# Optimization experiments

Hardware: AMD Instinct MI355X
Metric: run time of the kernel (lower is better)

The kernel has to match this reference:

```python
import jax, jax.numpy as jnp
import numpy as np

B, S, H, NH, L, MLP_MULT = 4, 1024, 1024, 16, 2, 4
DK = H // NH
EPS = 1e-5


def setup_inputs() -> dict:
    key = jax.random.key(0)
    ks = jax.random.split(key, 8)
    p = lambda k, shape: jax.random.normal(k, shape, dtype=jnp.float32) * 0.02
    return {
        'hidden_states': jax.random.normal(ks[0], (B, S, H), dtype=jnp.float32),
        'attn_w': p(ks[1], (L, H, 3 * H)),
        'attn_b': jnp.zeros((L, 3 * H), jnp.float32),
        'proj_w': p(ks[2], (L, H, H)),
        'proj_b': jnp.zeros((L, H), jnp.float32),
        'fc_w': p(ks[3], (L, H, MLP_MULT * H)),
        'fc_b': jnp.zeros((L, MLP_MULT * H), jnp.float32),
        'fc2_w': p(ks[4], (L, MLP_MULT * H, H)),
        'fc2_b': jnp.zeros((L, H), jnp.float32),
        'ln1_g': jnp.ones((L, H), jnp.float32),
        'ln1_b': jnp.zeros((L, H), jnp.float32),
        'ln2_g': jnp.ones((L, H), jnp.float32),
        'ln2_b': jnp.zeros((L, H), jnp.float32),
        'position_ids': jnp.arange(S, dtype=jnp.int32),
    }


def _ln(x, g, b):
    m = jnp.mean(x, axis=-1, keepdims=True)
    v = jnp.var(x, axis=-1, keepdims=True)
    return (x - m) * jax.lax.rsqrt(v + EPS) * g + b


def _rotate_half(x):
    x1, x2 = jnp.split(x, 2, axis=-1)
    return jnp.concatenate((-x2, x1), axis=-1)


def _forward(hidden_states, attn_w, attn_b, proj_w, proj_b, fc_w, fc_b,
             fc2_w, fc2_b, ln1_g, ln1_b, ln2_g, ln2_b, position_ids):
    # rotary tables (fp32 math, as in RotaryEmbedding.forward)
    inv_freq = 1.0 / (10000.0 ** (jnp.arange(0, DK, 2, dtype=jnp.float32) / DK))
    freqs = position_ids.astype(jnp.float32)[:, None] * inv_freq[None, :]  # [S, DK/2]
    emb = jnp.concatenate((freqs, freqs), axis=-1)                          # [S, DK]
    cos = jnp.cos(emb)[None, None]  # [1,1,S,DK]
    sin = jnp.sin(emb)[None, None]
    causal = jnp.tril(jnp.ones((S, S), dtype=bool))
    neg = jnp.finfo(jnp.float32).min
    scale = 1.0 / np.sqrt(DK).astype(np.float32)

    h = hidden_states
    for i in range(L):
        # attention block
        x = _ln(h, ln1_g[i], ln1_b[i])
        qkv = x @ attn_w[i] + attn_b[i]                  # Conv1D c_attn
        q, k, v = jnp.split(qkv, 3, axis=-1)
        heads = lambda t: t.reshape(B, S, NH, DK).transpose(0, 2, 1, 3)
        q, k, v = heads(q), heads(k), heads(v)           # [B,NH,S,DK]
        q = q * cos + _rotate_half(q) * sin
        k = k * cos + _rotate_half(k) * sin
        # fp32 QK^T (baddbmm with alpha=scale, beta=0)
        w = jnp.einsum('bhqd,bhkd->bhqk', q.astype(jnp.float32),
                       k.astype(jnp.float32)) * scale    # [B,NH,S,S]
        w = jnp.where(causal, w, neg)
        w = jax.nn.softmax(w, axis=-1).astype(v.dtype)   # attn dropout is identity (eval)
        a = jnp.einsum('bhqk,bhkd->bhqd', w, v)
        a = a.transpose(0, 2, 1, 3).reshape(B, S, H)     # merge_heads
        h = h + (a @ proj_w[i] + proj_b[i])              # c_proj + residual
        # MLP block (gelu_new == tanh-approx gelu)
        x = _ln(h, ln2_g[i], ln2_b[i])
        mid = jax.nn.gelu(x @ fc_w[i] + fc_b[i], approximate=True)
        h = h + (mid @ fc2_w[i] + fc2_b[i])
    return h


def reference(hidden_states, attn_w, attn_b, proj_w, proj_b, fc_w, fc_b,
              fc2_w, fc2_b, ln1_g, ln1_b, ln2_g, ln2_b, position_ids):
    return _forward(hidden_states, attn_w, attn_b, proj_w, proj_b, fc_w, fc_b,
                    fc2_w, fc2_b, ln1_g, ln1_b, ln2_g, ln2_b, position_ids)
```

## Files before the change

### kernel.cpp

```cpp
#include <hip/hip_runtime.h>

#define B_ 4
#define S_ 1024
#define H_ 1024
#define NH_ 16
#define DK_ 64
#define MLPH_ 4096
#define EPS_ 1e-5f

typedef __attribute__((ext_vector_type(8))) short short8_t;
typedef __attribute__((ext_vector_type(8))) unsigned short ushort8_t;
typedef __attribute__((ext_vector_type(4))) float f32x4;

__device__ __forceinline__ unsigned short f2bf(float f) {
  unsigned int u = __float_as_uint(f);
  u = u + 0x7fffu + ((u >> 16) & 1u);
  return (unsigned short)(u >> 16);
}
__device__ __forceinline__ float bf2f(unsigned short b) {
  return __uint_as_float(((unsigned int)b) << 16);
}

__device__ __forceinline__ void gload16(const void* g, void* l) {
  typedef const __attribute__((address_space(1))) unsigned int GU;
  typedef __attribute__((address_space(3))) unsigned int LU;
  __builtin_amdgcn_global_load_lds((GU*)(size_t)g, (LU*)(unsigned int)(size_t)l, 16, 0, 0);
}

__device__ __forceinline__ float gelu_tanh(float x) {
  float y = 1.5957691216057308f * (x + 0.044715f * x * x * x);
  return x / (1.0f + __expf(-y));
}

__global__ __launch_bounds__(256) void rope_tab_init(const int* __restrict__ pos,
                                                     float2* __restrict__ tab) {
  int idx = blockIdx.x * 256 + threadIdx.x;
  int d2 = idx & 31, s = idx >> 5;
  float invf = __expf(-0.2878231366242557f * (float)d2);
  float th = (float)pos[s] * invf;
  float sn, cs;
  __sincosf(th, &sn, &cs);
  tab[idx] = make_float2(cs, sn);
}

__global__ __launch_bounds__(256) void wconv(const float* __restrict__ src0,
                                             unsigned short* __restrict__ dst0,
                                             int K, int N) {
  __shared__ float t[32][33];
  const float* src = src0 + (size_t)blockIdx.z * K * N;
  unsigned short* dst = dst0 + (size_t)blockIdx.z * N * K;
  int n0 = blockIdx.x * 32, k0 = blockIdx.y * 32;
  int tid = threadIdx.x;
  int r = tid >> 3, c = (tid & 7) * 4;
  const float* s = src + (size_t)(k0 + r) * N + n0 + c;
  float4 v = *(const float4*)s;
  t[r][c] = v.x; t[r][c + 1] = v.y; t[r][c + 2] = v.z; t[r][c + 3] = v.w;
  __syncthreads();
  ushort4 o;
  o.x = f2bf(t[c + 0][r]); o.y = f2bf(t[c + 1][r]);
  o.z = f2bf(t[c + 2][r]); o.w = f2bf(t[c + 3][r]);
  *(ushort4*)(dst + (size_t)(n0 + r) * K + k0 + c) = o;
}

__global__ __launch_bounds__(256) void ln_kernel(const float* __restrict__ x,
                                                 const float* __restrict__ g,
                                                 const float* __restrict__ b,
                                                 unsigned short* __restrict__ y) {
  int row = blockIdx.x, tid = threadIdx.x;
  const float* xp = x + (size_t)row * H_;
  float4 v = *((const float4*)xp + tid);
  float s  = v.x + v.y + v.z + v.w;
  float s2 = v.x * v.x + v.y * v.y + v.z * v.z + v.w * v.w;
  #pragma unroll
  for (int o = 1; o < 64; o <<= 1) {
    s  += __shfl_xor(s, o, 64);
    s2 += __shfl_xor(s2, o, 64);
  }
  __shared__ float r1[4], r2[4];
  if ((tid & 63) == 0) { r1[tid >> 6] = s; r2[tid >> 6] = s2; }
  __syncthreads();
  s  = r1[0] + r1[1] + r1[2] + r1[3];
  s2 = r2[0] + r2[1] + r2[2] + r2[3];
  float mean = s * (1.0f / H_);
  float var  = s2 * (1.0f / H_) - mean * mean;
  float inv  = rsqrtf(var + EPS_);
  float4 gv = *((const float4*)g + tid);
  float4 bv = *((const float4*)b + tid);
  ushort4 o;
  o.x = f2bf((v.x - mean) * inv * gv.x + bv.x);
  o.y = f2bf((v.y - mean) * inv * gv.y + bv.y);
  o.z = f2bf((v.z - mean) * inv * gv.z + bv.z);
  o.w = f2bf((v.w - mean) * inv * gv.w + bv.w);
  *(ushort4*)(y + (size_t)row * H_ + tid * 4) = o;
}

template <int MODE, int NT>
__global__ __launch_bounds__(256) void gemm_mfma(
    const unsigned short* __restrict__ A, const unsigned short* __restrict__ Bt,
    const float* __restrict__ bias, const float* __restrict__ resid,
    void* __restrict__ outp, int M, int N, int K, const float2* __restrict__ rtab) {
  constexpr int BN = NT * 32;
  constexpr int CB = BN / 32;
  __shared__ __align__(16) unsigned short As[2][128 * 64];
  __shared__ __align__(16) unsigned short Bs[2][BN * 64];
  int tid = threadIdx.x;
  int w = tid >> 6, lane = tid & 63;
  int gx = gridDim.x;
  int bid = blockIdx.y * gx + blockIdx.x;
  int xcd = bid & 7, r = bid >> 3;
  int rw = gx >> 1;
  int ry = xcd >> 1, rx = xcd & 1;
  int lm = r / rw, ln = r % rw;
  int m0 = (ry * (gridDim.y >> 2) + lm) * 128;
  int n0 = (rx * rw + ln) * BN;
  int wr = w >> 1, wc = w & 1;
  int fr = lane & 15, kg = lane >> 4;
  f32x4 acc[4][NT];
  #pragma unroll
  for (int m = 0; m < 4; m++)
    #pragma unroll
    for (int n = 0; n < NT; n++) {
      acc[m][n][0] = 0.f; acc[m][n][1] = 0.f; acc[m][n][2] = 0.f; acc[m][n][3] = 0.f;
    }
  int srow = lane >> 3;
  int scol = ((lane & 7) ^ srow) * 8;
  const unsigned short* Ap = A  + (size_t)(m0 + w * 32 + srow) * K + scol;
  const unsigned short* Bp = Bt + (size_t)(n0 + w * (8 * CB) + srow) * K + scol;
  int sx = (fr & 7);
  int nk = K >> 6;
  {
    char* AsB = (char*)As[0] + w * 4096;
    char* BsB = (char*)Bs[0] + w * CB * 1024;
    #pragma unroll
    for (int i = 0; i < 4; i++) gload16(Ap + (size_t)i * 8 * K, AsB + i * 1024);
    #pragma unroll
    for (int i = 0; i < CB; i++) gload16(Bp + (size_t)i * 8 * K, BsB + i * 1024);
  }
  __syncthreads();
  for (int t = 0; t < nk; t++) {
    int cur = t & 1;
    if (t + 1 < nk) {
      const unsigned short* Ap2 = Ap + (size_t)(t + 1) * 64;
      const unsigned short* Bp2 = Bp + (size_t)(t + 1) * 64;
      char* AsB = (char*)As[cur ^ 1] + w * 4096;
      char* BsB = (char*)Bs[cur ^ 1] + w * CB * 1024;
      #pragma unroll
      for (int i = 0; i < 4; i++) gload16(Ap2 + (size_t)i * 8 * K, AsB + i * 1024);
      #pragma unroll
      for (int i = 0; i < CB; i++) gload16(Bp2 + (size_t)i * 8 * K, BsB + i * 1024);
    }
    #pragma unroll
    for (int kk = 0; kk < 2; kk++) {
      int slot = ((kk * 4 + kg) ^ sx) << 4;
      short8_t af[4], bfr[NT];
      #pragma unroll
      for (int m = 0; m < 4; m++)
        af[m] = *(const short8_t*)((char*)As[cur] + (wr * 64 + m * 16 + fr) * 128 + slot);
      #pragma unroll
      for (int n = 0; n < NT; n++)
        bfr[n] = *(const short8_t*)((char*)Bs[cur] + (wc * (NT * 16) + n * 16 + fr) * 128 + slot);
      #pragma unroll
      for (int m = 0; m < 4; m++)
        #pragma unroll
        for (int n = 0; n < NT; n++)
          acc[m][n] = __builtin_amdgcn_mfma_f32_16x16x32_bf16(af[m], bfr[n], acc[m][n], 0, 0, 0);
    }
    __syncthreads();
  }

  if (MODE == 3) {
    int seg = n0 >> 10;
    if (seg < 2) {
      #pragma unroll
      for (int n = 0; n < 2; n++) {
        int col0 = n0 + wc * 64 + n * 16 + fr;
        int d2 = n * 16 + fr;
        float bv0 = bias[col0], bv2 = bias[col0 + 32];
        #pragma unroll
        for (int m = 0; m < 4; m++) {
          int row = m0 + wr * 64 + m * 16 + kg * 4;
          #pragma unroll
          for (int r2 = 0; r2 < 4; r2++) {
            int s = (row + r2) & (S_ - 1);
            float2 cssn = rtab[(s << 5) + d2];
            float a0 = acc[m][n][r2] + bv0;
            float a2 = acc[m][n + 2][r2] + bv2;
            size_t base = (size_t)(row + r2) * N;
            ((unsigned short*)outp)[base + col0]      = f2bf(a0 * cssn.x - a2 * cssn.y);
            ((unsigned short*)outp)[base + col0 + 32] = f2bf(a2 * cssn.x + a0 * cssn.y);
          }
        }
      }
    } else {
      #pragma unroll
      for (int n = 0; n < NT; n++) {
        int col = n0 + wc * (NT * 16) + n * 16 + fr;
        float bv = bias[col];
        #pragma unroll
        for (int m = 0; m < 4; m++) {
          int row = m0 + wr * 64 + m * 16 + kg * 4;
          #pragma unroll
          for (int r2 = 0; r2 < 4; r2++)
            ((unsigned short*)outp)[(size_t)(row + r2) * N + col] = f2bf(acc[m][n][r2] + bv);
        }
      }
    }
    return;
  }
  #pragma unroll
  for (int n = 0; n < NT; n++) {
    int col = n0 + wc * (NT * 16) + n * 16 + fr;
    float bv = bias[col];
    #pragma unroll
    for (int m = 0; m < 4; m++) {
      int row = m0 + wr * 64 + m * 16 + kg * 4;
      #pragma unroll
      for (int r2 = 0; r2 < 4; r2++) {
        float v = acc[m][n][r2] + bv;
        size_t idx = (size_t)(row + r2) * N + col;
        if (MODE == 2)      ((float*)outp)[idx] = resid[idx] + v;
        else if (MODE == 1) ((unsigned short*)outp)[idx] = f2bf(gelu_tanh(v));
        else                ((unsigned short*)outp)[idx] = f2bf(v);
      }
    }
  }
}

__global__ __launch_bounds__(256) void attn9(const unsigned short* __restrict__ qkv,
                                             unsigned short* __restrict__ aout) {
  __shared__ __align__(16) unsigned short Ks[2][64 * 64];
  __shared__ __align__(16) unsigned short Vt[2][64 * 64];
  __shared__ __align__(16) unsigned short Ps[4][16 * 64];
  const float SCL2 = 0.18033688011112443f;
  const float THR2 = 11.541560327111708f;
  int tid = threadIdx.x;
  int w = tid >> 6, lane = tid & 63;
  int fr = lane & 15, kg = lane >> 4;
  int lid = ((blockIdx.z << 4) + blockIdx.y) * 16 + blockIdx.x;
  int phase = lid >> 8, s256 = lid & 255;
  int i = s256 >> 6, combo = s256 & 63;
  int qt;
  if (phase == 0)      qt = 15 - i;
  else if (phase == 1) qt = i;
  else if (phase == 2) qt = 11 - i;
  else                 qt = 4 + i;
  int head = combo & 15, b = combo >> 4;
  int q0 = qt * 64;
  const unsigned short* base = qkv + ((size_t)b * S_) * 3072 + head * 64;

  const unsigned short* qp = base + (size_t)(q0 + w * 16 + fr) * 3072 + kg * 8;
  short8_t qa0 = *(const short8_t*)qp;
  short8_t qa1 = *(const short8_t*)(qp + 32);

  f32x4 acc[4];
  float mrun = -3.0e38f, lrun = 0.f;
  #pragma unroll
  for (int n = 0; n < 4; n++) {
    acc[n][0] = 0.f; acc[n][1] = 0.f; acc[n][2] = 0.f; acc[n][3] = 0.f;
  }

  int skv = lane;
  int sd0 = w * 16;
  int qrow = q0 + w * 16 + fr;

  const unsigned short* kp0 = base + 1024 + (size_t)skv * 3072 + sd0;
  short8_t ka = *(const short8_t*)kp0;
  short8_t kb = *(const short8_t*)(kp0 + 8);
  short8_t va = *(const short8_t*)(kp0 + 1024);
  short8_t vb = *(const short8_t*)(kp0 + 1032);

  int ntiles = qt + 1;
  for (int t = 0; t < ntiles; t++) {
    int cur = t & 1;
    {
      unsigned kbyte = skv * 128 + sd0 * 2;
      unsigned ksw = (skv & 7) << 4;
      *(short8_t*)((char*)Ks[cur] + (kbyte ^ ksw)) = ka;
      *(short8_t*)((char*)Ks[cur] + ((kbyte + 16) ^ ksw)) = kb;
      #pragma unroll
      for (int j = 0; j < 8; j++) {
        int d0 = sd0 + j, d1 = sd0 + 8 + j;
        *(unsigned short*)((char*)Vt[cur] + ((d0 * 128 + skv * 2) ^ ((d0 & 7) << 4))) = (unsigned short)va[j];
        *(unsigned short*)((char*)Vt[cur] + ((d1 * 128 + skv * 2) ^ ((d1 & 7) << 4))) = (unsigned short)vb[j];
      }
    }
    if (t + 1 < ntiles) {
      const unsigned short* kp = base + 1024 + (size_t)((t + 1) * 64 + skv) * 3072 + sd0;
      ka = *(const short8_t*)kp;
      kb = *(const short8_t*)(kp + 8);
      va = *(const short8_t*)(kp + 1024);
      vb = *(const short8_t*)(kp + 1032);
    }
    __syncthreads();
    short8_t b0[4], b1[4], v0[4], v1[4];
    #pragma unroll
    for (int n = 0; n < 4; n++) {
      int kvrow = n * 16 + fr;
      unsigned sw = (kvrow & 7) << 4;
      b0[n] = *(const short8_t*)((char*)Ks[cur] + ((kvrow * 128 + kg * 16) ^ sw));
      b1[n] = *(const short8_t*)((char*)Ks[cur] + ((kvrow * 128 + 64 + kg * 16) ^ sw));
    }
    #pragma unroll
    for (int n = 0; n < 4; n++) {
      int d = n * 16 + fr;
      unsigned sw = (d & 7) << 4;
      v0[n] = *(const short8_t*)((char*)Vt[cur] + ((d * 128 + kg * 16) ^ sw));
      v1[n] = *(const short8_t*)((char*)Vt[cur] + ((d * 128 + 64 + kg * 16) ^ sw));
    }
    f32x4 st[4];
    __builtin_amdgcn_s_setprio(1);
    #pragma unroll
    for (int n = 0; n < 4; n++) {
      f32x4 z; z[0] = 0.f; z[1] = 0.f; z[2] = 0.f; z[3] = 0.f;
      z = __builtin_amdgcn_mfma_f32_16x16x32_bf16(b0[n], qa0, z, 0, 0, 0);
      z = __builtin_amdgcn_mfma_f32_16x16x32_bf16(b1[n], qa1, z, 0, 0, 0);
      st[n] = z;
    }
    __builtin_amdgcn_s_setprio(0);
    bool diag = (t == qt);
    float rm = -3.0e38f;
    #pragma unroll
    for (int n = 0; n < 4; n++)
      #pragma unroll
      for (int j = 0; j < 4; j++) {
        float sv = st[n][j] * SCL2;
        if (diag && (t * 64 + n * 16 + kg * 4 + j > qrow)) sv = -1.0e30f;
        st[n][j] = sv;
        rm = fmaxf(rm, sv);
      }
    if (__any(rm > mrun + THR2)) {
      rm = fmaxf(rm, __shfl_xor(rm, 16, 64));
      rm = fmaxf(rm, __shfl_xor(rm, 32, 64));
      float mn = fmaxf(mrun, rm);
      float sc = exp2f(mrun - mn);
      mrun = mn;
      lrun *= sc;
      #pragma unroll
      for (int n = 0; n < 4; n++) {
        acc[n][0] *= sc; acc[n][1] *= sc; acc[n][2] *= sc; acc[n][3] *= sc;
      }
    }
    {
      float ls = 0.f;
      #pragma unroll
      for (int n = 0; n < 4; n++) {
        float e0 = exp2f(st[n][0] - mrun);
        float e1 = exp2f(st[n][1] - mrun);
        float e2 = exp2f(st[n][2] - mrun);
        float e3 = exp2f(st[n][3] - mrun);
        ls += (e0 + e1) + (e2 + e3);
        unsigned lo, hi;
        asm("v_cvt_pk_bf16_f32 %0, %1, %2" : "=v"(lo) : "v"(e0), "v"(e1));
        asm("v_cvt_pk_bf16_f32 %0, %1, %2" : "=v"(hi) : "v"(e2), "v"(e3));
        uint2 pk; pk.x = lo; pk.y = hi;
        *(uint2*)((char*)Ps[w] + ((fr * 128 + n * 32 + kg * 8) ^ ((fr & 7) << 4))) = pk;
      }
      lrun += ls;
    }
    asm volatile("s_waitcnt lgkmcnt(0)" ::: "memory");
    unsigned psw = (fr & 7) << 4;
    short8_t pa0 = *(const short8_t*)((char*)Ps[w] + ((fr * 128 + kg * 16) ^ psw));
    short8_t pa1 = *(const short8_t*)((char*)Ps[w] + ((fr * 128 + 64 + kg * 16) ^ psw));
    __builtin_amdgcn_s_setprio(1);
    #pragma unroll
    for (int n = 0; n < 4; n++) {
      acc[n] = __builtin_amdgcn_mfma_f32_16x16x32_bf16(v0[n], pa0, acc[n], 0, 0, 0);
      acc[n] = __builtin_amdgcn_mfma_f32_16x16x32_bf16(v1[n], pa1, acc[n], 0, 0, 0);
    }
    __builtin_amdgcn_s_setprio(0);
  }
  {
    float ls = lrun;
    ls += __shfl_xor(ls, 16, 64);
    ls += __shfl_xor(ls, 32, 64);
    float inv = 1.0f / ls;
    size_t row = (size_t)b * S_ + q0 + w * 16 + fr;
    unsigned short* op = aout + row * H_ + head * 64 + kg * 4;
    #pragma unroll
    for (int n = 0; n < 4; n++) {
      ushort4 o;
      o.x = f2bf(acc[n][0] * inv);
      o.y = f2bf(acc[n][1] * inv);
      o.z = f2bf(acc[n][2] * inv);
      o.w = f2bf(acc[n][3] * inv);
      *(ushort4*)(op + n * 16) = o;
    }
  }
}

extern "C" void kernel_launch(void* const* d_in, const int* in_sizes, int n_in,
                              void* d_out, int out_size, void* d_ws, size_t ws_size,
                              hipStream_t stream) {
  const float* hs     = (const float*)d_in[0];
  const float* attn_w = (const float*)d_in[1];
  const float* attn_b = (const float*)d_in[2];
  const float* proj_w = (const float*)d_in[3];
  const float* proj_b = (const float*)d_in[4];
  const float* fc_w   = (const float*)d_in[5];
  const float* fc_b   = (const float*)d_in[6];
  const float* fc2_w  = (const float*)d_in[7];
  const float* fc2_b  = (const float*)d_in[8];
  const float* ln1_g  = (const float*)d_in[9];
  const float* ln1_b  = (const float*)d_in[10];
  const float* ln2_g  = (const float*)d_in[11];
  const float* ln2_b  = (const float*)d_in[12];
  const int*   pos    = (const int*)d_in[13];

  float* hres = (float*)d_out;
  const size_t rows = (size_t)B_ * S_;

  unsigned short* wQ    = (unsigned short*)d_ws;
  unsigned short* wP    = wQ  + (size_t)2 * 3072 * 1024;
  unsigned short* wF1   = wP  + (size_t)2 * 1024 * 1024;
  unsigned short* wF2   = wF1 + (size_t)2 * 4096 * 1024;
  unsigned short* xbf   = wF2 + (size_t)2 * 1024 * 4096;
  unsigned short* qkvbf = xbf + rows * H_;
  unsigned short* midbf = qkvbf + rows * 3 * H_;
  unsigned short* aoutbf= midbf + rows * MLPH_;
  float2* rtab = (float2*)(aoutbf + rows * H_);

  rope_tab_init<<<128, 256, 0, stream>>>(pos, rtab);
  wconv<<<dim3(96, 32, 2), 256, 0, stream>>>(attn_w, wQ, 1024, 3072);
  wconv<<<dim3(32, 32, 2), 256, 0, stream>>>(proj_w, wP, 1024, 1024);
  wconv<<<dim3(128, 32, 2), 256, 0, stream>>>(fc_w, wF1, 1024, 4096);
  wconv<<<dim3(32, 128, 2), 256, 0, stream>>>(fc2_w, wF2, 4096, 1024);

  for (int l = 0; l < 2; l++) {
    const float* hin = (l == 0) ? hs : hres;
    ln_kernel<<<rows, 256, 0, stream>>>(hin, ln1_g + l * H_, ln1_b + l * H_, xbf);
    gemm_mfma<3, 4><<<dim3(24, 32), 256, 0, stream>>>(
        xbf, wQ + (size_t)l * 3072 * 1024, attn_b + (size_t)l * 3072, nullptr,
        qkvbf, 4096, 3072, 1024, rtab);
    attn9<<<dim3(16, 16, 4), 256, 0, stream>>>(qkvbf, aoutbf);
    gemm_mfma<2, 2><<<dim3(16, 32), 256, 0, stream>>>(
        aoutbf, wP + (size_t)l * 1024 * 1024, proj_b + (size_t)l * 1024, hin,
        hres, 4096, 1024, 1024, nullptr);
    ln_kernel<<<rows, 256, 0, stream>>>(hres, ln2_g + l * H_, ln2_b + l * H_, xbf);
    gemm_mfma<1, 4><<<dim3(32, 32), 256, 0, stream>>>(
        xbf, wF1 + (size_t)l * 4096 * 1024, fc_b + (size_t)l * 4096, nullptr,
        midbf, 4096, 4096, 1024, nullptr);
    gemm_mfma<2, 2><<<dim3(16, 32), 256, 0, stream>>>(
        midbf, wF2 + (size_t)l * 1024 * 4096, fc2_b + (size_t)l * 1024, hres,
        hres, 4096, 1024, 4096, nullptr);
  }
}
```

Measured before the change: 405.4 us.

## Rewrite GEMM with prefetch-two-ahead pipeline, larger tiles and 8-wave blocks

Replaces the double-buffered GEMM with a version that keeps two K-stages in flight. Fragments are loaded into registers before the barrier so the next-next stage can be issued into the buffer just freed, with explicit vmcnt waits in place of __syncthreads. It also widens each wave's tile to 64x64, uses 8-wave (512-thread) blocks for the QKV and FC1 GEMMs with a 256-wide N tile, and raises MFMA priority around the compute loop. The intent is to hide global-load latency and raise reuse per block. In exchange the grids are smaller, register pressure is higher, and correctness depends on hand-counted vmcnt values.

```diff
diff --git a/kernel.cpp b/kernel.cpp
--- a/kernel.cpp
+++ b/kernel.cpp
@@ -94,17 +94,23 @@
   *(ushort4*)(y + (size_t)row * H_ + tid * 4) = o;
 }
 
-template <int MODE, int NT>
-__global__ __launch_bounds__(256) void gemm_mfma(
+template <int MODE, int WAVES>
+__global__ __launch_bounds__(WAVES * 64) void gemm_pipe(
     const unsigned short* __restrict__ A, const unsigned short* __restrict__ Bt,
     const float* __restrict__ bias, const float* __restrict__ resid,
     void* __restrict__ outp, int M, int N, int K, const float2* __restrict__ rtab) {
-  constexpr int BN = NT * 32;
-  constexpr int CB = BN / 32;
-  __shared__ __align__(16) unsigned short As[2][128 * 64];
-  __shared__ __align__(16) unsigned short Bs[2][BN * 64];
+  constexpr int WC = WAVES / 2;
+  constexpr int BN = WC * 64;
+  constexpr int NCH = 16 + WC * 8;
+  constexpr int CPW = NCH / WAVES;
+  constexpr int ABYTES = 128 * 128;
+  constexpr int BUFSZ = (16 + WC * 8) * 1024;
+  __shared__ __align__(16) char Ls[2 * BUFSZ];
   int tid = threadIdx.x;
   int w = tid >> 6, lane = tid & 63;
+  int wr = w / WC, wc = w % WC;
+  int fr = lane & 15, kg = lane >> 4;
+  int sx = fr & 7;
   int gx = gridDim.x;
   int bid = blockIdx.y * gx + blockIdx.x;
   int xcd = bid & 7, r = bid >> 3;
@@ -113,60 +119,79 @@
   int lm = r / rw, ln = r % rw;
   int m0 = (ry * (gridDim.y >> 2) + lm) * 128;
   int n0 = (rx * rw + ln) * BN;
-  int wr = w >> 1, wc = w & 1;
-  int fr = lane & 15, kg = lane >> 4;
-  f32x4 acc[4][NT];
+
+  f32x4 acc[4][4];
   #pragma unroll
   for (int m = 0; m < 4; m++)
     #pragma unroll
-    for (int n = 0; n < NT; n++) {
+    for (int n = 0; n < 4; n++) {
       acc[m][n][0] = 0.f; acc[m][n][1] = 0.f; acc[m][n][2] = 0.f; acc[m][n][3] = 0.f;
     }
+
   int srow = lane >> 3;
   int scol = ((lane & 7) ^ srow) * 8;
-  const unsigned short* Ap = A  + (size_t)(m0 + w * 32 + srow) * K + scol;
-  const unsigned short* Bp = Bt + (size_t)(n0 + w * (8 * CB) + srow) * K + scol;
-  int sx = (fr & 7);
+  const unsigned short* sbase[CPW];
+  int soff[CPW];
+  #pragma unroll
+  for (int i = 0; i < CPW; i++) {
+    int c = w * CPW + i;
+    sbase[i] = (c < 16) ? A  + (size_t)(m0 + c * 8 + srow) * K + scol
+                        : Bt + (size_t)(n0 + (c - 16) * 8 + srow) * K + scol;
+    soff[i] = c * 1024;
+  }
   int nk = K >> 6;
-  {
-    char* AsB = (char*)As[0] + w * 4096;
-    char* BsB = (char*)Bs[0] + w * CB * 1024;
-    #pragma unroll
-    for (int i = 0; i < 4; i++) gload16(Ap + (size_t)i * 8 * K, AsB + i * 1024);
-    #pragma unroll
-    for (int i = 0; i < CB; i++) gload16(Bp + (size_t)i * 8 * K, BsB + i * 1024);
-  }
-  __syncthreads();
+
+  #define STAGE_(tk, bsel)                                                   \
+    {                                                                        \
+      _Pragma("unroll")                                                      \
+      for (int i = 0; i < CPW; i++)                                          \
+        gload16(sbase[i] + (size_t)(tk) * 64, Ls + (bsel) * BUFSZ + soff[i]); \
+    }
+
+  STAGE_(0, 0);
+  STAGE_(1, 1);
+  if constexpr (WAVES == 8) asm volatile("s_waitcnt vmcnt(6)" ::: "memory");
+  else                      asm volatile("s_waitcnt vmcnt(8)" ::: "memory");
+  __builtin_amdgcn_s_barrier();
+
   for (int t = 0; t < nk; t++) {
-    int cur = t & 1;
-    if (t + 1 < nk) {
-      const unsigned short* Ap2 = Ap + (size_t)(t + 1) * 64;
-      const unsigned short* Bp2 = Bp + (size_t)(t + 1) * 64;
-      char* AsB = (char*)As[cur ^ 1] + w * 4096;
-      char* BsB = (char*)Bs[cur ^ 1] + w * CB * 1024;
-      #pragma unroll
-      for (int i = 0; i < 4; i++) gload16(Ap2 + (size_t)i * 8 * K, AsB + i * 1024);
-      #pragma unroll
-      for (int i = 0; i < CB; i++) gload16(Bp2 + (size_t)i * 8 * K, BsB + i * 1024);
-    }
-    #pragma unroll
-    for (int kk = 0; kk < 2; kk++) {
-      int slot = ((kk * 4 + kg) ^ sx) << 4;
-      short8_t af[4], bfr[NT];
-      #pragma unroll
-      for (int m = 0; m < 4; m++)
-        af[m] = *(const short8_t*)((char*)As[cur] + (wr * 64 + m * 16 + fr) * 128 + slot);
-      #pragma unroll
-      for (int n = 0; n < NT; n++)
-        bfr[n] = *(const short8_t*)((char*)Bs[cur] + (wc * (NT * 16) + n * 16 + fr) * 128 + slot);
+    const char* bufc = Ls + (t & 1) * BUFSZ;
+    short8_t af[4][2], bfv[4][2];
+    #pragma unroll
+    for (int m = 0; m < 4; m++) {
+      int row = wr * 64 + m * 16 + fr;
+      #pragma unroll
+      for (int kk = 0; kk < 2; kk++)
+        af[m][kk] = *(const short8_t*)(bufc + row * 128 + (((kk * 4 + kg) ^ sx) << 4));
+    }
+    #pragma unroll
+    for (int n = 0; n < 4; n++) {
+      int row = wc * 64 + n * 16 + fr;
+      #pragma unroll
+      for (int kk = 0; kk < 2; kk++)
+        bfv[n][kk] = *(const short8_t*)(bufc + ABYTES + row * 128 + (((kk * 4 + kg) ^ sx) << 4));
+    }
+    asm volatile("s_waitcnt lgkmcnt(0)" ::: "memory");
+    __builtin_amdgcn_s_barrier();
+    if (t + 2 < nk) STAGE_(t + 2, t & 1);
+    __builtin_amdgcn_s_setprio(1);
+    #pragma unroll
+    for (int kk = 0; kk < 2; kk++)
       #pragma unroll
       for (int m = 0; m < 4; m++)
         #pragma unroll
-        for (int n = 0; n < NT; n++)
-          acc[m][n] = __builtin_amdgcn_mfma_f32_16x16x32_bf16(af[m], bfr[n], acc[m][n], 0, 0, 0);
-    }
-    __syncthreads();
-  }
+        for (int n = 0; n < 4; n++)
+          acc[m][n] = __builtin_amdgcn_mfma_f32_16x16x32_bf16(af[m][kk], bfv[n][kk], acc[m][n], 0, 0, 0);
+    __builtin_amdgcn_s_setprio(0);
+    if (t + 2 < nk) {
+      if constexpr (WAVES == 8) asm volatile("s_waitcnt vmcnt(6)" ::: "memory");
+      else                      asm volatile("s_waitcnt vmcnt(8)" ::: "memory");
+    } else {
+      asm volatile("s_waitcnt vmcnt(0)" ::: "memory");
+    }
+    __builtin_amdgcn_s_barrier();
+  }
+  #undef STAGE_
 
   if (MODE == 3) {
     int seg = n0 >> 10;
@@ -193,8 +218,8 @@
       }
     } else {
       #pragma unroll
-      for (int n = 0; n < NT; n++) {
-        int col = n0 + wc * (NT * 16) + n * 16 + fr;
+      for (int n = 0; n < 4; n++) {
+        int col = n0 + wc * 64 + n * 16 + fr;
         float bv = bias[col];
         #pragma unroll
         for (int m = 0; m < 4; m++) {
@@ -208,8 +233,8 @@
     return;
   }
   #pragma unroll
-  for (int n = 0; n < NT; n++) {
-    int col = n0 + wc * (NT * 16) + n * 16 + fr;
+  for (int n = 0; n < 4; n++) {
+    int col = n0 + wc * 64 + n * 16 + fr;
     float bv = bias[col];
     #pragma unroll
     for (int m = 0; m < 4; m++) {
@@ -428,18 +453,18 @@
   for (int l = 0; l < 2; l++) {
     const float* hin = (l == 0) ? hs : hres;
     ln_kernel<<<rows, 256, 0, stream>>>(hin, ln1_g + l * H_, ln1_b + l * H_, xbf);
-    gemm_mfma<3, 4><<<dim3(24, 32), 256, 0, stream>>>(
+    gemm_pipe<3, 8><<<dim3(12, 32), 512, 0, stream>>>(
         xbf, wQ + (size_t)l * 3072 * 1024, attn_b + (size_t)l * 3072, nullptr,
         qkvbf, 4096, 3072, 1024, rtab);
     attn9<<<dim3(16, 16, 4), 256, 0, stream>>>(qkvbf, aoutbf);
-    gemm_mfma<2, 2><<<dim3(16, 32), 256, 0, stream>>>(
+    gemm_pipe<2, 4><<<dim3(8, 32), 256, 0, stream>>>(
         aoutbf, wP + (size_t)l * 1024 * 1024, proj_b + (size_t)l * 1024, hin,
         hres, 4096, 1024, 1024, nullptr);
     ln_kernel<<<rows, 256, 0, stream>>>(hres, ln2_g + l * H_, ln2_b + l * H_, xbf);
-    gemm_mfma<1, 4><<<dim3(32, 32), 256, 0, stream>>>(
+    gemm_pipe<1, 8><<<dim3(16, 32), 512, 0, stream>>>(
         xbf, wF1 + (size_t)l * 4096 * 1024, fc_b + (size_t)l * 4096, nullptr,
         midbf, 4096, 4096, 1024, nullptr);
-    gemm_mfma<2, 2><<<dim3(16, 32), 256, 0, stream>>>(
+    gemm_pipe<2, 4><<<dim3(8, 32), 256, 0, stream>>>(
         midbf, wF2 + (size_t)l * 1024 * 4096, fc2_b + (size_t)l * 1024, hres,
         hres, 4096, 1024, 4096, nullptr);
   }
```

Result: slower. 446.6 us (+10.2%).

## Halve GEMM K-tile to 32 with unified LDS buffer and new swizzle

Applied to the files above, without the earlier changes.

Reworks the MFMA GEMM main loop to stage K-slices of 32 instead of 64. A and B tiles now share one double-buffered LDS array, and loads are redistributed as 16-row chunks across the four waves with a 4-way XOR swizzle. This halves shared memory per block, which may raise occupancy. In exchange it doubles the number of loop iterations and __syncthreads barriers per GEMM and leaves less load/compute overlap per stage.

```diff
diff --git a/kernel.cpp b/kernel.cpp
--- a/kernel.cpp
+++ b/kernel.cpp
@@ -100,9 +100,11 @@
     const float* __restrict__ bias, const float* __restrict__ resid,
     void* __restrict__ outp, int M, int N, int K, const float2* __restrict__ rtab) {
   constexpr int BN = NT * 32;
-  constexpr int CB = BN / 32;
-  __shared__ __align__(16) unsigned short As[2][128 * 64];
-  __shared__ __align__(16) unsigned short Bs[2][BN * 64];
+  constexpr int ACH = 8;
+  constexpr int NCH = 8 + NT * 2;
+  constexpr int CPW = NCH / 4;
+  constexpr int BUFSZ = NCH * 1024;
+  __shared__ __align__(16) char Ls[2 * BUFSZ];
   int tid = threadIdx.x;
   int w = tid >> 6, lane = tid & 63;
   int gx = gridDim.x;
@@ -122,51 +124,49 @@
     for (int n = 0; n < NT; n++) {
       acc[m][n][0] = 0.f; acc[m][n][1] = 0.f; acc[m][n][2] = 0.f; acc[m][n][3] = 0.f;
     }
-  int srow = lane >> 3;
-  int scol = ((lane & 7) ^ srow) * 8;
-  const unsigned short* Ap = A  + (size_t)(m0 + w * 32 + srow) * K + scol;
-  const unsigned short* Bp = Bt + (size_t)(n0 + w * (8 * CB) + srow) * K + scol;
-  int sx = (fr & 7);
-  int nk = K >> 6;
-  {
-    char* AsB = (char*)As[0] + w * 4096;
-    char* BsB = (char*)Bs[0] + w * CB * 1024;
-    #pragma unroll
-    for (int i = 0; i < 4; i++) gload16(Ap + (size_t)i * 8 * K, AsB + i * 1024);
-    #pragma unroll
-    for (int i = 0; i < CB; i++) gload16(Bp + (size_t)i * 8 * K, BsB + i * 1024);
-  }
+  int srow = lane >> 2;
+  int scol = ((lane & 3) ^ (srow & 3)) * 8;
+  const unsigned short* sbase[CPW];
+  int soff[CPW];
+  #pragma unroll
+  for (int i = 0; i < CPW; i++) {
+    int c = w * CPW + i;
+    sbase[i] = (c < ACH) ? A  + (size_t)(m0 + c * 16 + srow) * K + scol
+                         : Bt + (size_t)(n0 + (c - ACH) * 16 + srow) * K + scol;
+    soff[i] = c * 1024;
+  }
+  int rsl = (fr & 3);
+  int nk = K >> 5;
+
+  #define STAGE_(tk, bsel)                                                     \
+    {                                                                          \
+      _Pragma("unroll")                                                        \
+      for (int i = 0; i < CPW; i++)                                            \
+        gload16(sbase[i] + (size_t)(tk) * 32, Ls + (bsel) * BUFSZ + soff[i]);  \
+    }
+
+  STAGE_(0, 0);
   __syncthreads();
   for (int t = 0; t < nk; t++) {
     int cur = t & 1;
-    if (t + 1 < nk) {
-      const unsigned short* Ap2 = Ap + (size_t)(t + 1) * 64;
-      const unsigned short* Bp2 = Bp + (size_t)(t + 1) * 64;
-      char* AsB = (char*)As[cur ^ 1] + w * 4096;
-      char* BsB = (char*)Bs[cur ^ 1] + w * CB * 1024;
-      #pragma unroll
-      for (int i = 0; i < 4; i++) gload16(Ap2 + (size_t)i * 8 * K, AsB + i * 1024);
-      #pragma unroll
-      for (int i = 0; i < CB; i++) gload16(Bp2 + (size_t)i * 8 * K, BsB + i * 1024);
-    }
-    #pragma unroll
-    for (int kk = 0; kk < 2; kk++) {
-      int slot = ((kk * 4 + kg) ^ sx) << 4;
-      short8_t af[4], bfr[NT];
-      #pragma unroll
-      for (int m = 0; m < 4; m++)
-        af[m] = *(const short8_t*)((char*)As[cur] + (wr * 64 + m * 16 + fr) * 128 + slot);
+    if (t + 1 < nk) STAGE_(t + 1, cur ^ 1);
+    const char* bufc = Ls + cur * BUFSZ;
+    int slot = (kg ^ rsl) << 4;
+    short8_t af[4], bfv[NT];
+    #pragma unroll
+    for (int m = 0; m < 4; m++)
+      af[m] = *(const short8_t*)(bufc + (wr * 64 + m * 16 + fr) * 64 + slot);
+    #pragma unroll
+    for (int n = 0; n < NT; n++)
+      bfv[n] = *(const short8_t*)(bufc + ACH * 1024 + (wc * (NT * 16) + n * 16 + fr) * 64 + slot);
+    #pragma unroll
+    for (int m = 0; m < 4; m++)
       #pragma unroll
       for (int n = 0; n < NT; n++)
-        bfr[n] = *(const short8_t*)((char*)Bs[cur] + (wc * (NT * 16) + n * 16 + fr) * 128 + slot);
-      #pragma unroll
-      for (int m = 0; m < 4; m++)
-        #pragma unroll
-        for (int n = 0; n < NT; n++)
-          acc[m][n] = __builtin_amdgcn_mfma_f32_16x16x32_bf16(af[m], bfr[n], acc[m][n], 0, 0, 0);
-    }
+        acc[m][n] = __builtin_amdgcn_mfma_f32_16x16x32_bf16(af[m], bfv[n], acc[m][n], 0, 0, 0);
     __syncthreads();
   }
+  #undef STAGE_
 
   if (MODE == 3) {
     int seg = n0 >> 10;
```

After: 470.1 us. 1.16x slower.
